# Optimization experiments

Hardware: AMD Instinct MI355X
Metric: run time of the kernel (lower is better)

## Reference

```python
import jax, jax.numpy as jnp
import numpy as np

N_NODES = 100000


def gcn_conv(x, edge_index, W, b):
    """PyG GCNConv: out = D^-1/2 (A+I) D^-1/2 (X W) + b, edge weights = 1."""
    n = x.shape[0]
    h = x @ W  # [N, F_out]
    row, col = edge_index[0], edge_index[1]  # source -> target
    ones = jnp.ones(row.shape[0], dtype=x.dtype)
    # degree on A + I (self loop contributes 1)
    deg = jax.ops.segment_sum(ones, col, num_segments=n) + 1.0
    dinv = jax.lax.rsqrt(deg)  # deg >= 1 so no inf
    norm = dinv[row] * dinv[col]  # [E]
    agg = jax.ops.segment_sum(h[row] * norm[:, None], col, num_segments=n)
    agg = agg + h * (dinv * dinv)[:, None]  # self-loop term
    return agg + b


def setup_inputs() -> dict:
    key = jax.random.key(0)
    ks = jax.random.split(key, 8)
    E = 3200000
    F_in, H, C = 128, 16, 2
    x = jax.random.normal(ks[0], (N_NODES, F_in), dtype=jnp.float32)
    edge_index = jax.random.randint(ks[1], (2, E), 0, N_NODES, dtype=jnp.int64)
    W1 = jax.random.normal(ks[2], (F_in, H), dtype=jnp.float32) * (1.0 / np.sqrt(F_in))
    b1 = jnp.zeros((H,), jnp.float32)
    W2 = jax.random.normal(ks[3], (H, H), dtype=jnp.float32) * (1.0 / np.sqrt(H))
    b2 = jnp.zeros((H,), jnp.float32)
    fc1_W = jax.random.normal(ks[4], (2 * H, H), dtype=jnp.float32) * (1.0 / np.sqrt(2 * H))
    fc1_b = jnp.zeros((H,), jnp.float32)
    fc2_W = jax.random.normal(ks[5], (H, C), dtype=jnp.float32) * (1.0 / np.sqrt(H))
    fc2_b = jnp.zeros((C,), jnp.float32)
    return {"x": x, "edge_index": edge_index, "W1": W1, "b1": b1, "W2": W2,
            "b2": b2, "fc1_W": fc1_W, "fc1_b": fc1_b, "fc2_W": fc2_W, "fc2_b": fc2_b}


def reference(x, edge_index, W1, b1, W2, b2, fc1_W, fc1_b, fc2_W, fc2_b):
    h = jax.nn.relu(gcn_conv(x, edge_index, W1, b1))
    h = jax.nn.relu(gcn_conv(h, edge_index, W2, b2))
    row, col = edge_index[0], edge_index[1]
    ef = jnp.concatenate([h[row], h[col]], axis=1)  # [E, 32]
    ef = jax.nn.relu(ef @ fc1_W + fc1_b)
    logits = ef @ fc2_W + fc2_b  # [E, 2]
    return jax.nn.log_softmax(logits, axis=1)
```

## Files before the change

### kernel.cpp

```cpp
#include <hip/hip_runtime.h>
#include <hip/hip_fp16.h>
#include <cstdint>
#include <cstddef>

#define F_IN 128
#define HID 16
#define NBUK 1024
#define NPB  128
#define CHUNK 8192
#define CHUNK2 16384

typedef float f4v __attribute__((ext_vector_type(4)));
typedef float f2v __attribute__((ext_vector_type(2)));
typedef int   i2v __attribute__((ext_vector_type(2)));
typedef int   i4v __attribute__((ext_vector_type(4)));
typedef _Float16 h8 __attribute__((ext_vector_type(8)));

__global__ void k_detect(const int* __restrict__ eidx, int* __restrict__ flag) {
    if (blockIdx.x == 0 && threadIdx.x == 0) {
        int all0 = 1;
        for (int i = 0; i < 64; ++i) {
            if (eidx[2 * i + 1] != 0) { all0 = 0; break; }
        }
        *flag = all0;
    }
}

__device__ __forceinline__ int ld_idx_nt(const int* __restrict__ p, int e, int is64) {
    return is64 ? __builtin_nontemporal_load(&p[2 * e])
                : __builtin_nontemporal_load(&p[e]);
}

__launch_bounds__(256)
__global__ void k_bhist(const int* __restrict__ eidx, int E,
                        const int* __restrict__ flag, int* __restrict__ ghist) {
    __shared__ int lh[NBUK];
    int t = threadIdx.x;
    for (int i = t; i < NBUK; i += 256) lh[i] = 0;
    __syncthreads();
    int base = blockIdx.x * CHUNK;
    int cnt = min(CHUNK, E - base);
    int is64 = *flag;
    const int* colp = eidx + ((size_t)E << is64);
    for (int i = t; i < cnt; i += 256)
        atomicAdd(&lh[ld_idx_nt(colp, base + i, is64) >> 7], 1);
    __syncthreads();
    for (int i = t; i < NBUK; i += 256)
        if (lh[i]) atomicAdd(&ghist[i], lh[i]);
}

__global__ void k_bscan(const int* __restrict__ ghist, int E,
                        int* __restrict__ boff, int* __restrict__ gcur) {
    __shared__ int s[NBUK];
    int t = threadIdx.x;
    int v = ghist[t];
    s[t] = v;
    __syncthreads();
    for (int off = 1; off < NBUK; off <<= 1) {
        int a = (t >= off) ? s[t - off] : 0;
        __syncthreads();
        s[t] += a;
        __syncthreads();
    }
    int excl = s[t] - v;
    boff[t] = excl;
    gcur[t] = excl;
    if (t == NBUK - 1) boff[NBUK] = E;
}

__launch_bounds__(512)
__global__ void k_bscatter(const int* __restrict__ eidx, int E,
                           const int* __restrict__ flag,
                           int* __restrict__ gcur, uint32_t* __restrict__ pairs) {
    __shared__ int lh[NBUK];
    __shared__ int lcur[NBUK];
    int t = threadIdx.x;
    for (int i = t; i < NBUK; i += 512) lh[i] = 0;
    __syncthreads();
    int base = blockIdx.x * CHUNK2;
    int cnt = min(CHUNK2, E - base);
    int is64 = *flag;
    const int* rowp = eidx;
    const int* colp = eidx + ((size_t)E << is64);
    for (int i = t; i < cnt; i += 512)
        atomicAdd(&lh[ld_idx_nt(colp, base + i, is64) >> 7], 1);
    __syncthreads();
    for (int i = t; i < NBUK; i += 512) {
        int c = lh[i];
        lcur[i] = c ? atomicAdd(&gcur[i], c) : 0;
    }
    __syncthreads();
    for (int i = t; i < cnt; i += 512) {
        int e = base + i;
        int c = ld_idx_nt(colp, e, is64);
        int r = ld_idx_nt(rowp, e, is64);
        int buk = c >> 7;
        int pos = atomicAdd(&lcur[buk], 1);
        pairs[pos] = (uint32_t)r | ((uint32_t)(c & (NPB - 1)) << 20);
    }
}

__launch_bounds__(256)
__global__ void k_bsort(const uint32_t* __restrict__ pairs, const int* __restrict__ boff,
                        int* __restrict__ srcs, int* __restrict__ noff,
                        float* __restrict__ dinv, int n) {
    __shared__ int cnt[NPB];
    __shared__ int scn[NPB];
    int t = threadIdx.x;
    int b = blockIdx.x;
    if (t < NPB) cnt[t] = 0;
    __syncthreads();
    int beg = boff[b], end = boff[b + 1];
    for (int k = beg + t; k < end; k += 256)
        atomicAdd(&cnt[pairs[k] >> 20], 1);
    __syncthreads();
    if (t < NPB) scn[t] = cnt[t];
    __syncthreads();
    for (int off = 1; off < NPB; off <<= 1) {
        int v = 0;
        if (t < NPB && t >= off) v = scn[t - off];
        __syncthreads();
        if (t < NPB) scn[t] += v;
        __syncthreads();
    }
    if (t < NPB) {
        int node = b * NPB + t;
        int excl = scn[t] - cnt[t];
        if (node <= n) noff[node] = beg + excl;
        if (node < n)  dinv[node] = rsqrtf((float)cnt[t] + 1.0f);
        cnt[t] = beg + excl;
    }
    __syncthreads();
    for (int k = beg + t; k < end; k += 256) {
        uint32_t p = pairs[k];
        int pos = atomicAdd(&cnt[p >> 20], 1);
        srcs[pos] = (int)(p & 0xFFFFF);
    }
}

__launch_bounds__(256)
__global__ void k_gemm1(const float* __restrict__ x, const float* __restrict__ W1,
                        const float* __restrict__ dinv, __half* __restrict__ hs, int n) {
    __shared__ float Wt[16 * 132];
    for (int i = threadIdx.x; i < F_IN * HID; i += 256) {
        int k = i >> 4, j = i & 15;
        Wt[j * 132 + k] = W1[i];
    }
    __syncthreads();
    int row = blockIdx.x * 16 + (threadIdx.x >> 4);
    int j = threadIdx.x & 15;
    if (row >= n) return;
    const f4v* xr = (const f4v*)(x + (size_t)row * F_IN);
    float acc = 0.f;
#pragma unroll
    for (int kk = 0; kk < 32; ++kk) {
        f4v xv = __builtin_nontemporal_load(&xr[kk]);
        float4 wv = *(const float4*)&Wt[j * 132 + 4 * kk];
        acc += xv.x * wv.x + xv.y * wv.y + xv.z * wv.z + xv.w * wv.w;
    }
    hs[(size_t)row * HID + j] = __float2half(acc * dinv[row]);
}

template <int EPI>
__launch_bounds__(256)
__global__ void k_layer(const int* __restrict__ srcs, const int* __restrict__ noff,
                        const __half* __restrict__ hs, const float* __restrict__ dinv,
                        const float* __restrict__ bias, const float* __restrict__ Wnext,
                        __half* __restrict__ out0) {
    __shared__ float Ws[256];
    __shared__ float bs[16];
    __shared__ float srow[16 * 17];
    int t = threadIdx.x;
    if (EPI == 0) { if (t < 256) Ws[t] = Wnext[t]; }
    if (t < 16) bs[t] = bias[t];
    __syncthreads();

    int i = blockIdx.x * 16 + (t >> 4);
    int j = t & 15;
    int beg = noff[i], end = noff[i + 1];
    float acc = __half2float(hs[(size_t)i * HID + j]);

    int kb = beg;
    for (; kb + 16 <= end; kb += 16) {
        int idx = __builtin_nontemporal_load(&srcs[kb + j]);
#pragma unroll
        for (int m = 0; m < 16; ++m) {
            int r = __shfl(idx, m, 16);
            acc += __half2float(hs[(size_t)r * HID + j]);
        }
    }
    if (kb < end) {
        int lim = end - kb;
        int idx = srcs[kb + ((j < lim) ? j : (lim - 1))];
        for (int m = 0; m < lim; ++m) {
            int r = __shfl(idx, m, 16);
            acc += __half2float(hs[(size_t)r * HID + j]);
        }
    }

    float di = dinv[i];
    float hrelu = fmaxf(acc * di + bs[j], 0.f);
    if (EPI == 1) {
        out0[(size_t)i * HID + j] = __float2half(hrelu);
        return;
    }
    int ln = t >> 4;
    srow[ln * 17 + j] = hrelu;
    __syncthreads();
    float a0 = 0.f;
#pragma unroll
    for (int k = 0; k < 16; ++k) a0 += srow[ln * 17 + k] * Ws[k * 16 + j];
    out0[(size_t)i * HID + j] = __float2half(a0 * di);
}

#define EDGE_ITER 8
__launch_bounds__(256)
__global__ void k_edge(const int* __restrict__ eidx, int E,
                       const int* __restrict__ flag,
                       const _Float16* __restrict__ h2,
                       const float* __restrict__ fc1W, const float* __restrict__ fc1b,
                       const float* __restrict__ fc2W, const float* __restrict__ fc2b,
                       float* __restrict__ out) {
    int t = threadIdx.x;
    int l = t & 63;
    int wv = t >> 6;
    int m = l & 15;
    int kb = l >> 4;
    int side = kb >> 1;
    int part = kb & 1;

    h8 bf;
#pragma unroll
    for (int j = 0; j < 8; ++j)
        bf[j] = (_Float16)fc1W[(8 * kb + j) * 16 + m];
    float b1v = fc1b[m];
    f4v cinit; cinit.x = b1v; cinit.y = b1v; cinit.z = b1v; cinit.w = b1v;
    float w20 = fc2W[2 * m], w21 = fc2W[2 * m + 1];
    float b20 = fc2b[0], b21 = fc2b[1];

    int is64 = *flag;
    const int* rowp = eidx;
    const int* colp = eidx + ((size_t)E << is64);
    const int* idxp = side ? colp : rowp;

    for (int it = 0; it < EDGE_ITER; ++it) {
        int grp = (blockIdx.x * EDGE_ITER + it) * 4 + wv;
        int base = grp * 16;
        if (base >= E) return;
        int eA = base + m;
        if (eA >= E) eA = E - 1;
        int node = ld_idx_nt(idxp, eA, is64);
        h8 av = *(const h8*)(h2 + (size_t)node * HID + part * 8);
        f4v z = __builtin_amdgcn_mfma_f32_16x16x32_f16(av, bf, cinit, 0, 0, 0);
        float l0[4], l1[4];
#pragma unroll
        for (int q = 0; q < 4; ++q) {
            float zr = fmaxf(z[q], 0.f);
            float v0 = zr * w20, v1 = zr * w21;
#pragma unroll
            for (int msk = 1; msk < 16; msk <<= 1) {
                v0 += __shfl_xor(v0, msk);
                v1 += __shfl_xor(v1, msk);
            }
            float a = b20 + v0, b = b21 + v1;
            float mm = fmaxf(a, b);
            float lse = mm + __logf(__expf(a - mm) + __expf(b - mm));
            l0[q] = a - lse; l1[q] = b - lse;
        }
        if (m == 0) {
            int e0 = base + kb * 4;
            if (e0 + 3 < E) {
                f4v o1; o1.x = l0[0]; o1.y = l1[0]; o1.z = l0[1]; o1.w = l1[1];
                f4v o2; o2.x = l0[2]; o2.y = l1[2]; o2.z = l0[3]; o2.w = l1[3];
                __builtin_nontemporal_store(o1, (f4v*)(out + 2 * (size_t)e0));
                __builtin_nontemporal_store(o2, (f4v*)(out + 2 * (size_t)e0 + 4));
            } else {
                for (int q = 0; q < 4; ++q) {
                    if (e0 + q < E) {
                        f2v o; o.x = l0[q]; o.y = l1[q];
                        __builtin_nontemporal_store(o, (f2v*)(out + 2 * (size_t)(e0 + q)));
                    }
                }
            }
        }
    }
}

static inline size_t rnd4(size_t v) { return (v + 3) & ~(size_t)3; }

extern "C" void kernel_launch(void* const* d_in, const int* in_sizes, int n_in,
                              void* d_out, int out_size, void* d_ws, size_t ws_size,
                              hipStream_t stream) {
    const float* x    = (const float*)d_in[0];
    const int*   eidx = (const int*)d_in[1];
    const float* W1   = (const float*)d_in[2];
    const float* b1   = (const float*)d_in[3];
    const float* W2   = (const float*)d_in[4];
    const float* b2   = (const float*)d_in[5];
    const float* fc1W = (const float*)d_in[6];
    const float* fc1b = (const float*)d_in[7];
    const float* fc2W = (const float*)d_in[8];
    const float* fc2b = (const float*)d_in[9];

    const int n = in_sizes[0] / F_IN;
    const int E = in_sizes[1] / 2;
    const int NBLK_HIST = (E + CHUNK - 1) / CHUNK;
    const int NBLK_SCAT = (E + CHUNK2 - 1) / CHUNK2;
    const int NBLK_BUK  = (n + NPB - 1) / NPB;

    float* ws = (float*)d_ws;
    size_t a = 0;
    float*    dinv  = ws + a;              a += rnd4(n);
    uint32_t* pairs = (uint32_t*)(ws + a); a += rnd4(E);
    int*      srcs  = (int*)(ws + a);      a += rnd4(E);
    int*      noff  = (int*)(ws + a);      a += rnd4(n + 1);
    int*      boff  = (int*)(ws + a);      a += rnd4(NBUK + 1);
    int*      gcur  = (int*)(ws + a);      a += NBUK;
    int*      ghist = (int*)(ws + a);      a += NBUK;
    int*      flag  = (int*)(ws + a);      a += 4;
    __half*   hs1   = (__half*)(ws + a);   a += rnd4((size_t)n * HID / 2);
    __half*   hs2   = (__half*)(ws + a);   a += rnd4((size_t)n * HID / 2);
    __half*   h2b   = (__half*)(ws + a);   a += rnd4((size_t)n * HID / 2);
    float* out = (float*)d_out;

    k_detect<<<1, 64, 0, stream>>>(eidx, flag);

    (void)hipMemsetAsync(ghist, 0, NBUK * sizeof(int), stream);
    k_bhist<<<NBLK_HIST, 256, 0, stream>>>(eidx, E, flag, ghist);
    k_bscan<<<1, NBUK, 0, stream>>>(ghist, E, boff, gcur);
    k_bscatter<<<NBLK_SCAT, 512, 0, stream>>>(eidx, E, flag, gcur, pairs);
    k_bsort<<<NBLK_BUK, 256, 0, stream>>>(pairs, boff, srcs, noff, dinv, n);

    k_gemm1<<<(n + 15) / 16, 256, 0, stream>>>(x, W1, dinv, hs1, n);

    k_layer<0><<<n / 16, 256, 0, stream>>>(srcs, noff, hs1, dinv, b1, W2, hs2);
    k_layer<1><<<n / 16, 256, 0, stream>>>(srcs, noff, hs2, dinv, b2, nullptr, h2b);
    {
        int ngrp = (E + 15) / 16;
        int nblk = (ngrp + 4 * EDGE_ITER - 1) / (4 * EDGE_ITER);
        k_edge<<<nblk, 256, 0, stream>>>(eidx, E, flag, (const _Float16*)h2b,
                                         fc1W, fc1b, fc2W, fc2b, out);
    }
}
```

Before: 319.6 us.

## Precompute per-block bucket offsets and transpose edge MFMA to cut shuffles

The histogram kernel now stores per-block bucket counts, and a new column-wise scan kernel turns them into per-block write offsets. This removes the second histogram pass and the global atomics from the scatter kernel. The edge kernel swaps the MFMA operands so each lane holds 4 hidden units of one edge, which reduces the fc2 reduction from 4x4 shuffle rounds to 2 shuffles. Costs are an extra kernel launch and a gcnt workspace array with strided reads, and the edge output is now written as per-lane 8-byte stores instead of 16-byte stores.

```diff
diff --git a/kernel.cpp b/kernel.cpp
--- a/kernel.cpp
+++ b/kernel.cpp
@@ -7,7 +7,6 @@
 #define HID 16
 #define NBUK 1024
 #define NPB  128
-#define CHUNK 8192
 #define CHUNK2 16384
 
 typedef float f4v __attribute__((ext_vector_type(4)));
@@ -31,26 +30,29 @@
                 : __builtin_nontemporal_load(&p[e]);
 }
 
-__launch_bounds__(256)
+__launch_bounds__(512)
 __global__ void k_bhist(const int* __restrict__ eidx, int E,
-                        const int* __restrict__ flag, int* __restrict__ ghist) {
+                        const int* __restrict__ flag, int* __restrict__ ghist,
+                        int* __restrict__ gcnt) {
     __shared__ int lh[NBUK];
     int t = threadIdx.x;
-    for (int i = t; i < NBUK; i += 256) lh[i] = 0;
-    __syncthreads();
-    int base = blockIdx.x * CHUNK;
-    int cnt = min(CHUNK, E - base);
+    for (int i = t; i < NBUK; i += 512) lh[i] = 0;
+    __syncthreads();
+    int base = blockIdx.x * CHUNK2;
+    int cnt = min(CHUNK2, E - base);
     int is64 = *flag;
     const int* colp = eidx + ((size_t)E << is64);
-    for (int i = t; i < cnt; i += 256)
+    for (int i = t; i < cnt; i += 512)
         atomicAdd(&lh[ld_idx_nt(colp, base + i, is64) >> 7], 1);
     __syncthreads();
-    for (int i = t; i < NBUK; i += 256)
-        if (lh[i]) atomicAdd(&ghist[i], lh[i]);
-}
-
-__global__ void k_bscan(const int* __restrict__ ghist, int E,
-                        int* __restrict__ boff, int* __restrict__ gcur) {
+    for (int i = t; i < NBUK; i += 512) {
+        int v = lh[i];
+        gcnt[(size_t)blockIdx.x * NBUK + i] = v;
+        if (v) atomicAdd(&ghist[i], v);
+    }
+}
+
+__global__ void k_bscan(const int* __restrict__ ghist, int E, int* __restrict__ boff) {
     __shared__ int s[NBUK];
     int t = threadIdx.x;
     int v = ghist[t];
@@ -62,34 +64,41 @@
         s[t] += a;
         __syncthreads();
     }
-    int excl = s[t] - v;
-    boff[t] = excl;
-    gcur[t] = excl;
+    boff[t] = s[t] - v;
     if (t == NBUK - 1) boff[NBUK] = E;
+}
+
+__launch_bounds__(512)
+__global__ void k_bscan2(int* __restrict__ gcnt, const int* __restrict__ boff, int nb) {
+    __shared__ int s[512];
+    int t = threadIdx.x;
+    int k = blockIdx.x;
+    int v = (t < nb) ? gcnt[(size_t)t * NBUK + k] : 0;
+    s[t] = v;
+    __syncthreads();
+    for (int off = 1; off < 512; off <<= 1) {
+        int a = (t >= off) ? s[t - off] : 0;
+        __syncthreads();
+        s[t] += a;
+        __syncthreads();
+    }
+    if (t < nb) gcnt[(size_t)t * NBUK + k] = boff[k] + (s[t] - v);
 }
 
 __launch_bounds__(512)
 __global__ void k_bscatter(const int* __restrict__ eidx, int E,
                            const int* __restrict__ flag,
-                           int* __restrict__ gcur, uint32_t* __restrict__ pairs) {
-    __shared__ int lh[NBUK];
+                           const int* __restrict__ gcnt, uint32_t* __restrict__ pairs) {
     __shared__ int lcur[NBUK];
     int t = threadIdx.x;
-    for (int i = t; i < NBUK; i += 512) lh[i] = 0;
+    for (int i = t; i < NBUK; i += 512)
+        lcur[i] = gcnt[(size_t)blockIdx.x * NBUK + i];
     __syncthreads();
     int base = blockIdx.x * CHUNK2;
     int cnt = min(CHUNK2, E - base);
     int is64 = *flag;
     const int* rowp = eidx;
     const int* colp = eidx + ((size_t)E << is64);
-    for (int i = t; i < cnt; i += 512)
-        atomicAdd(&lh[ld_idx_nt(colp, base + i, is64) >> 7], 1);
-    __syncthreads();
-    for (int i = t; i < NBUK; i += 512) {
-        int c = lh[i];
-        lcur[i] = c ? atomicAdd(&gcur[i], c) : 0;
-    }
-    __syncthreads();
     for (int i = t; i < cnt; i += 512) {
         int e = base + i;
         int c = ld_idx_nt(colp, e, is64);
@@ -225,17 +234,23 @@
     int l = t & 63;
     int wv = t >> 6;
     int m = l & 15;
-    int kb = l >> 4;
-    int side = kb >> 1;
-    int part = kb & 1;
-
-    h8 bf;
+    int g = l >> 4;
+    int side = g >> 1;
+    int part = g & 1;
+
+    h8 af;
 #pragma unroll
     for (int j = 0; j < 8; ++j)
-        bf[j] = (_Float16)fc1W[(8 * kb + j) * 16 + m];
-    float b1v = fc1b[m];
-    f4v cinit; cinit.x = b1v; cinit.y = b1v; cinit.z = b1v; cinit.w = b1v;
-    float w20 = fc2W[2 * m], w21 = fc2W[2 * m + 1];
+        af[j] = (_Float16)fc1W[(8 * g + j) * 16 + m];
+    f4v cinit;
+#pragma unroll
+    for (int q = 0; q < 4; ++q) cinit[q] = fc1b[4 * g + q];
+    float w2x[4], w2y[4];
+#pragma unroll
+    for (int q = 0; q < 4; ++q) {
+        w2x[q] = fc2W[(4 * g + q) * 2];
+        w2y[q] = fc2W[(4 * g + q) * 2 + 1];
+    }
     float b20 = fc2b[0], b21 = fc2b[1];
 
     int is64 = *flag;
@@ -250,38 +265,23 @@
         int eA = base + m;
         if (eA >= E) eA = E - 1;
         int node = ld_idx_nt(idxp, eA, is64);
-        h8 av = *(const h8*)(h2 + (size_t)node * HID + part * 8);
-        f4v z = __builtin_amdgcn_mfma_f32_16x16x32_f16(av, bf, cinit, 0, 0, 0);
-        float l0[4], l1[4];
+        h8 bv = *(const h8*)(h2 + (size_t)node * HID + part * 8);
+        f4v z = __builtin_amdgcn_mfma_f32_16x16x32_f16(af, bv, cinit, 0, 0, 0);
+        float v0 = 0.f, v1 = 0.f;
 #pragma unroll
         for (int q = 0; q < 4; ++q) {
             float zr = fmaxf(z[q], 0.f);
-            float v0 = zr * w20, v1 = zr * w21;
-#pragma unroll
-            for (int msk = 1; msk < 16; msk <<= 1) {
-                v0 += __shfl_xor(v0, msk);
-                v1 += __shfl_xor(v1, msk);
-            }
-            float a = b20 + v0, b = b21 + v1;
-            float mm = fmaxf(a, b);
-            float lse = mm + __logf(__expf(a - mm) + __expf(b - mm));
-            l0[q] = a - lse; l1[q] = b - lse;
-        }
-        if (m == 0) {
-            int e0 = base + kb * 4;
-            if (e0 + 3 < E) {
-                f4v o1; o1.x = l0[0]; o1.y = l1[0]; o1.z = l0[1]; o1.w = l1[1];
-                f4v o2; o2.x = l0[2]; o2.y = l1[2]; o2.z = l0[3]; o2.w = l1[3];
-                __builtin_nontemporal_store(o1, (f4v*)(out + 2 * (size_t)e0));
-                __builtin_nontemporal_store(o2, (f4v*)(out + 2 * (size_t)e0 + 4));
-            } else {
-                for (int q = 0; q < 4; ++q) {
-                    if (e0 + q < E) {
-                        f2v o; o.x = l0[q]; o.y = l1[q];
-                        __builtin_nontemporal_store(o, (f2v*)(out + 2 * (size_t)(e0 + q)));
-                    }
-                }
-            }
+            v0 += zr * w2x[q];
+            v1 += zr * w2y[q];
+        }
+        v0 += __shfl_xor(v0, 16); v0 += __shfl_xor(v0, 32);
+        v1 += __shfl_xor(v1, 16); v1 += __shfl_xor(v1, 32);
+        float a = b20 + v0, b = b21 + v1;
+        float mm = fmaxf(a, b);
+        float lse = mm + __logf(__expf(a - mm) + __expf(b - mm));
+        if (g == 0 && base + m < E) {
+            f2v res; res.x = a - lse; res.y = b - lse;
+            __builtin_nontemporal_store(res, (f2v*)(out + 2 * (size_t)(base + m)));
         }
     }
 }
@@ -304,7 +304,6 @@
 
     const int n = in_sizes[0] / F_IN;
     const int E = in_sizes[1] / 2;
-    const int NBLK_HIST = (E + CHUNK - 1) / CHUNK;
     const int NBLK_SCAT = (E + CHUNK2 - 1) / CHUNK2;
     const int NBLK_BUK  = (n + NPB - 1) / NPB;
 
@@ -315,9 +314,9 @@
     int*      srcs  = (int*)(ws + a);      a += rnd4(E);
     int*      noff  = (int*)(ws + a);      a += rnd4(n + 1);
     int*      boff  = (int*)(ws + a);      a += rnd4(NBUK + 1);
-    int*      gcur  = (int*)(ws + a);      a += NBUK;
     int*      ghist = (int*)(ws + a);      a += NBUK;
     int*      flag  = (int*)(ws + a);      a += 4;
+    int*      gcnt  = (int*)(ws + a);      a += rnd4((size_t)NBLK_SCAT * NBUK);
     __half*   hs1   = (__half*)(ws + a);   a += rnd4((size_t)n * HID / 2);
     __half*   hs2   = (__half*)(ws + a);   a += rnd4((size_t)n * HID / 2);
     __half*   h2b   = (__half*)(ws + a);   a += rnd4((size_t)n * HID / 2);
@@ -326,9 +325,10 @@
     k_detect<<<1, 64, 0, stream>>>(eidx, flag);
 
     (void)hipMemsetAsync(ghist, 0, NBUK * sizeof(int), stream);
-    k_bhist<<<NBLK_HIST, 256, 0, stream>>>(eidx, E, flag, ghist);
-    k_bscan<<<1, NBUK, 0, stream>>>(ghist, E, boff, gcur);
-    k_bscatter<<<NBLK_SCAT, 512, 0, stream>>>(eidx, E, flag, gcur, pairs);
+    k_bhist<<<NBLK_SCAT, 512, 0, stream>>>(eidx, E, flag, ghist, gcnt);
+    k_bscan<<<1, NBUK, 0, stream>>>(ghist, E, boff);
+    k_bscan2<<<NBUK, 512, 0, stream>>>(gcnt, boff, NBLK_SCAT);
+    k_bscatter<<<NBLK_SCAT, 512, 0, stream>>>(eidx, E, flag, gcnt, pairs);
     k_bsort<<<NBLK_BUK, 256, 0, stream>>>(pairs, boff, srcs, noff, dinv, n);
 
     k_gemm1<<<(n + 15) / 16, 256, 0, stream>>>(x, W1, dinv, hs1, n);
```

New measurement: 288.1 us. 1.11x faster.
